# Kernel tuning notes

Hardware: AMD Instinct MI355X
Metric: run time of the kernel (lower is better)

The kernel has to match this reference:

```python
import jax, jax.numpy as jnp
import numpy as np
from jax import lax

B, CIN, COUT, H, W = 16, 256, 128, 32, 32
KD = 3   # deformable conv kernel
KU = 4
PAD = 1  # deform conv padding
EPS = 1e-5


def setup_inputs() -> dict:
    key = jax.random.key(0)
    ks = jax.random.split(key, 5)
    s3 = 1.0 / np.sqrt(CIN * KD * KD)
    s_up = 1.0 / np.sqrt(COUT * KU * KU)
    return {
        "x": jax.random.normal(ks[0], (B, CIN, H, W), jnp.float32),
        "w_off": jax.random.normal(ks[1], (3 * KD * KD, CIN, KD, KD), jnp.float32) * s3,
        "b_off": jnp.zeros((3 * KD * KD,), jnp.float32),
        "w_dcn": jax.random.normal(ks[2], (COUT, CIN, KD, KD), jnp.float32) * s3,
        "b_dcn": jnp.zeros((COUT,), jnp.float32),
        "g1": jnp.ones((COUT,), jnp.float32),
        "bt1": jnp.zeros((COUT,), jnp.float32),
        "w_up": jax.random.normal(ks[3], (COUT, COUT, KU, KU), jnp.float32) * s_up,  # torch ConvTranspose2d weight layout (in, out, kh, kw)
        "g2": jnp.ones((COUT,), jnp.float32),
        "bt2": jnp.zeros((COUT,), jnp.float32),
    }


def _conv3x3(x, w, b):
    y = lax.conv_general_dilated(x, w, (1, 1), [(1, 1), (1, 1)],
                                 dimension_numbers=("NCHW", "OIHW", "NCHW"))
    return y + b[None, :, None, None]


def _bn_relu(x, g, b):
    # training-mode BatchNorm2d: batch stats over (N, H, W), biased variance
    mu = jnp.mean(x, (0, 2, 3), keepdims=True)
    var = jnp.var(x, (0, 2, 3), keepdims=True)
    y = (x - mu) * lax.rsqrt(var + EPS)
    return jax.nn.relu(y * g[None, :, None, None] + b[None, :, None, None])


def _deform_conv(x, offset, mask, w, b):
    # modulated deformable conv v2, matching torchvision.ops.DeformConv2d
    Bb, C, Hh, Ww = x.shape
    Kk = KD * KD
    off = offset.reshape(Bb, Kk, 2, Hh, Ww)
    dy, dx = off[:, :, 0], off[:, :, 1]          # [B, Kk, H, W]
    ky, kx = jnp.meshgrid(jnp.arange(KD), jnp.arange(KD), indexing="ij")
    ky = (ky.reshape(-1) - PAD).astype(x.dtype)  # [Kk]
    kx = (kx.reshape(-1) - PAD).astype(x.dtype)
    ii = jnp.arange(Hh, dtype=x.dtype)[None, None, :, None]
    jj = jnp.arange(Ww, dtype=x.dtype)[None, None, None, :]
    py = ii + ky[None, :, None, None] + dy       # [B, Kk, H, W] sample rows
    px = jj + kx[None, :, None, None] + dx       # [B, Kk, H, W] sample cols
    y0 = jnp.floor(py)
    x0 = jnp.floor(px)
    wy = py - y0
    wx = px - x0
    HW = Hh * Ww
    x_flat = x.reshape(Bb, 1, C, HW)

    def corner(yc, xc, wgt):
        valid = (yc >= 0) & (yc <= Hh - 1) & (xc >= 0) & (xc <= Ww - 1)
        yi = jnp.clip(yc, 0, Hh - 1).astype(jnp.int32)
        xi = jnp.clip(xc, 0, Ww - 1).astype(jnp.int32)
        idx = (yi * Ww + xi).reshape(Bb, Kk, 1, HW)
        v = jnp.take_along_axis(x_flat, jnp.broadcast_to(idx, (Bb, Kk, C, HW)), axis=-1)
        wv = (wgt * valid.astype(x.dtype)).reshape(Bb, Kk, 1, HW)
        return v * wv

    samp = (corner(y0, x0, (1 - wy) * (1 - wx)) + corner(y0, x0 + 1, (1 - wy) * wx)
            + corner(y0 + 1, x0, wy * (1 - wx)) + corner(y0 + 1, x0 + 1, wy * wx))
    samp = samp * mask.reshape(Bb, Kk, 1, HW)    # [B, Kk, C, HW]
    out = jnp.einsum("bkcp,ock->bop", samp, w.reshape(w.shape[0], C, Kk))
    return out.reshape(Bb, -1, Hh, Ww) + b[None, :, None, None]


def reference(x, w_off, b_off, w_dcn, b_dcn, g1, bt1, w_up, g2, bt2):
    off = _conv3x3(x, w_off, b_off)              # [B, 27, H, W]
    Kk = KD * KD
    o1, o2, m = off[:, :Kk], off[:, Kk:2 * Kk], off[:, 2 * Kk:]
    offset = jnp.concatenate([o1, o2], axis=1)   # [B, 18, H, W], torchvision pair layout
    mask = jax.nn.sigmoid(m)
    y = _deform_conv(x, offset, mask, w_dcn, b_dcn)
    y = _bn_relu(y, g1, bt1)
    # ConvTranspose2d(k=4, s=2, p=1): conv over lhs-dilated input with flipped kernel
    w_t = jnp.flip(w_up, (2, 3)).transpose(1, 0, 2, 3)  # (out, in, kh, kw)
    p = KU - 1 - 1  # k - 1 - deconv_pad
    y = lax.conv_general_dilated(y, w_t, (1, 1), [(p, p), (p, p)],
                                 lhs_dilation=(2, 2),
                                 dimension_numbers=("NCHW", "OIHW", "NCHW"))
    return _bn_relu(y, g2, bt2)
```

## Files before the change

### kernel.cpp

```cpp
#include <hip/hip_runtime.h>
#include <hip/hip_fp16.h>
#include <math.h>

#define HW 1024
#define EPSV 1e-5f

typedef unsigned int uint;
typedef unsigned short ushort;
typedef __attribute__((ext_vector_type(8))) short short8;
typedef __attribute__((ext_vector_type(8))) _Float16 half8;
typedef __attribute__((ext_vector_type(4))) float floatx4;

static const size_t BOFF = 0;
static const size_t BD   = 36864;
static const size_t BQ   = 184320;
static const size_t XT   = 315392;
static const size_t OFFB = 2412544;
static const size_t ST1  = 2936832;
static const size_t ST2  = 2937856;
static const size_t YP   = 2941952;
static const size_t YSUM = 7136256;
static const size_t YBN  = 8184832;
static const size_t OB   = 9233408;

__device__ inline ushort f2bf(float f) {
  uint u = __builtin_bit_cast(uint, f);
  uint r = (u + 0x7FFFu + ((u >> 16) & 1u)) >> 16;
  return (ushort)r;
}
__device__ inline float b2f(ushort u) {
  return __builtin_bit_cast(float, ((uint)u) << 16);
}

__global__ __launch_bounds__(256) void prep_xt_kernel(const float* __restrict__ x,
                                                      const float* __restrict__ w_off,
                                                      const float* __restrict__ w_dcn,
                                                      const float* __restrict__ w_up,
                                                      float* __restrict__ ws) {
  __shared__ float tile[64 * 65];
  int blk = blockIdx.x;
  int tid = threadIdx.x;
  if (blk < 1024) {
    int b = blk & 15, pt = (blk >> 4) & 15, cc = blk >> 8;
    int p0 = pt * 64, c0 = cc * 64;
    int pp4 = tid & 15, ci = tid >> 4;
#pragma unroll
    for (int it = 0; it < 4; ++it) {
      int c = it * 16 + ci;
      float4 v = *(const float4*)(x + ((size_t)(b * 256 + c0 + c)) * HW + p0 + pp4 * 4);
      tile[c * 65 + pp4 * 4 + 0] = v.x;
      tile[c * 65 + pp4 * 4 + 1] = v.y;
      tile[c * 65 + pp4 * 4 + 2] = v.z;
      tile[c * 65 + pp4 * 4 + 3] = v.w;
    }
    __syncthreads();
    int cp = tid & 31, pp2 = tid >> 5;
    uint* xtu = (uint*)(ws + XT);
#pragma unroll
    for (int it = 0; it < 8; ++it) {
      int p = it * 8 + pp2;
      __half2 h = __floats2half2_rn(tile[(2 * cp) * 65 + p], tile[(2 * cp + 1) * 65 + p]);
      xtu[(size_t)(b * 1024 + p0 + p) * 128 + cc * 32 + cp] = __builtin_bit_cast(uint, h);
    }
  } else if (blk < 3488) {
    int i = (blk - 1024) * 256 + tid;
    if (i < 73728) {
      int j = i & 7;
      int lane = (i >> 3) & 63;
      int nh = (i >> 9) & 1;
      int k2 = (i >> 10) & 3;
      int cs = (i >> 12) & 1;
      int tap = i >> 13;
      int n = nh * 16 + (lane & 15);
      int c = cs * 128 + k2 * 32 + (lane >> 4) * 8 + j;
      float v = (n < 27) ? w_off[((size_t)n * 256 + c) * 9 + tap] : 0.f;
      ((__half*)(ws + BOFF))[i] = __float2half(v);
    } else if (i < 73728 + 294912) {
      int d = i - 73728;
      int oc = d / 2304; int k = d % 2304;
      int tap = k >> 8; int c = k & 255;
      ((__half*)(ws + BD))[d] = __float2half(w_dcn[((size_t)oc * 256 + c) * 9 + tap]);
    } else if (i < 73728 + 294912 + 262144) {
      int d = i - (73728 + 294912);
      int j = d & 7; int n = (d >> 3) & 127; int quad = (d >> 10) & 3;
      int kstep = (d >> 12) & 15; int par = d >> 16;
      int k = kstep * 32 + quad * 8 + j;
      int t4 = k >> 7; int c = k & 127;
      int ty = t4 >> 1, tx = t4 & 1;
      int pu = par >> 1, pv = par & 1;
      int ky = (1 - pu) + 2 * ty, kx = (1 - pv) + 2 * tx;
      float v = w_up[((size_t)c * 128 + n) * 16 + ky * 4 + kx];
      ((ushort*)(ws + BQ))[d] = f2bf(v);
    }
  } else {
    int i = (blk - 3488) * 256 + tid;
    if (i < 5120) ws[ST1 + i] = 0.f;
    else if (i < 5120 + 524288) ws[OFFB + (i - 5120)] = 0.f;
  }
}

__global__ __launch_bounds__(256) void offconv_mfma_kernel(const __half* __restrict__ xt,
                                                           const __half* __restrict__ bofr,
                                                           float* __restrict__ off) {
  __shared__ short As[102 * 132];
  int blk = blockIdx.x;
  int b = blk & 15, cs = (blk >> 4) & 1, pt = blk >> 5;
  int h = pt;
  int tid = threadIdx.x;
  int wid = tid >> 6, lane = tid & 63, lr = lane & 15, quad = lane >> 4;
  int m_w = (wid & 1) * 16, nh = wid >> 1;
  int n_w = nh * 16;
  const __half* xb = xt + (size_t)b * 1024 * 256 + cs * 128;

  for (int idx = tid; idx < 1632; idx += 256) {
    int pos = idx >> 4, seg = idx & 15;
    int r = pos / 34, jj = pos - r * 34;
    int ig = min(max(h - 1 + r, 0), 31);
    int jg = min(max(jj - 1, 0), 31);
    const float4* src = (const float4*)(xb + (size_t)(ig * 32 + jg) * 256 + seg * 8);
    *(float4*)(As + pos * 132 + seg * 8) = *src;
  }
  __syncthreads();

  floatx4 acc = (floatx4)0.f;
  int m = m_w + lr;
  const __half* bb = bofr + (size_t)lane * 8;
#pragma unroll
  for (int tap = 0; tap < 9; ++tap) {
    int ty = tap / 3, tx = tap % 3;
    bool valid = (h + ty - 1 >= 0) && (h + ty - 1 <= 31) && (m + tx - 1 >= 0) && (m + tx - 1 <= 31);
    int apos = (ty * 34 + m + tx) * 132;
#pragma unroll
    for (int k2 = 0; k2 < 4; ++k2) {
      short8 a = *(const short8*)(As + apos + k2 * 32 + quad * 8);
      short8 az = valid ? a : (short8)0;
      half8 af = __builtin_bit_cast(half8, az);
      half8 bf = *(const half8*)(bb + (size_t)((((tap * 2 + cs) * 4 + k2) * 2) + nh) * 512);
      acc = __builtin_amdgcn_mfma_f32_16x16x32_f16(af, bf, acc, 0, 0, 0);
    }
  }
  int n = n_w + lr;
#pragma unroll
  for (int r = 0; r < 4; ++r) {
    int mm = m_w + quad * 4 + r;
    atomicAdd(&off[((size_t)(b * 1024 + pt * 32 + mm)) * 32 + n], acc[r]);
  }
}

__global__ __launch_bounds__(256, 8) void deform_mfma_kernel(const __half* __restrict__ xt,
                                                             const float* __restrict__ off,
                                                             const float* __restrict__ b_off,
                                                             const __half* __restrict__ bd,
                                                             ushort* __restrict__ y_part) {
  __shared__ short As[64 * 72];
  __shared__ short Bs[128 * 72];
  int blk = blockIdx.x;
  int b = blk & 15;
  int rr = blk >> 4;
  int ptile = rr & 15, cs = rr >> 4;
  int tid = threadIdx.x;
  int wid = tid >> 6, lane = tid & 63, lr = lane & 15, quad = lane >> 4;
  int m_w = (wid & 1) * 32, n_w = (wid >> 1) * 64;
  int P0 = ptile * 64;
  int pix_l = tid >> 2, cseg = tid & 3;
  int pix = P0 + pix_l;
  int h = pix >> 5, w = pix & 31;
  const float* offb = off + (size_t)(b * 1024 + pix) * 32;
  const __half* xb = xt + (size_t)b * 1024 * 256 + cs * 64 + cseg * 16;
  int ocb = tid >> 1, seg = tid & 1;
  const __half* bdr = bd + (size_t)ocb * 2304 + cs * 64 + seg * 32;

  floatx4 acc[2][4];
#pragma unroll
  for (int mi = 0; mi < 2; ++mi)
#pragma unroll
    for (int ni = 0; ni < 4; ++ni) acc[mi][ni] = (floatx4)0.f;

#pragma unroll
  for (int tap = 0; tap < 9; ++tap) {
    float2 dn = *(const float2*)(offb + 2 * tap);
    float mr = offb[18 + tap];
    float dy = dn.x + b_off[2 * tap];
    float dx = dn.y + b_off[2 * tap + 1];
    float mraw = mr + b_off[18 + tap];
    float mm = 1.f / (1.f + __expf(-mraw));
    float py = (float)(h + tap / 3 - 1) + dy;
    float px = (float)(w + tap % 3 - 1) + dx;
    float y0f = floorf(py), x0f = floorf(px);
    float wy = py - y0f, wx = px - x0f;
    int y0 = (int)y0f, x0 = (int)x0f;
    float cw[4] = {(1.f - wy) * (1.f - wx), (1.f - wy) * wx, wy * (1.f - wx), wy * wx};
    uint4 q[4][2];
    __half2 w2[4];
#pragma unroll
    for (int t = 0; t < 4; ++t) {
      int yy = y0 + (t >> 1), xx = x0 + (t & 1);
      bool v = (yy >= 0) && (yy <= 31) && (xx >= 0) && (xx <= 31);
      int yc = min(max(yy, 0), 31), xc = min(max(xx, 0), 31);
      const uint4* xr = (const uint4*)(xb + (size_t)(yc * 32 + xc) * 256);
      q[t][0] = xr[0]; q[t][1] = xr[1];
      w2[t] = __float2half2_rn(v ? cw[t] * mm : 0.f);
    }
    const float4* gb = (const float4*)(bdr + tap * 256);
    float4 b0 = gb[0], b1 = gb[1], b2 = gb[2], b3 = gb[3];

    __half2 hacc[8];
#pragma unroll
    for (int j = 0; j < 8; ++j) hacc[j] = __float2half2_rn(0.f);
#pragma unroll
    for (int t = 0; t < 4; ++t) {
      uint qa[8] = {q[t][0].x, q[t][0].y, q[t][0].z, q[t][0].w,
                    q[t][1].x, q[t][1].y, q[t][1].z, q[t][1].w};
#pragma unroll
      for (int j = 0; j < 8; ++j)
        hacc[j] = __hfma2(w2[t], __builtin_bit_cast(__half2, qa[j]), hacc[j]);
    }
    if (tap) __syncthreads();
    {
      float4 f0, f1;
      f0.x = __builtin_bit_cast(float, hacc[0]);
      f0.y = __builtin_bit_cast(float, hacc[1]);
      f0.z = __builtin_bit_cast(float, hacc[2]);
      f0.w = __builtin_bit_cast(float, hacc[3]);
      f1.x = __builtin_bit_cast(float, hacc[4]);
      f1.y = __builtin_bit_cast(float, hacc[5]);
      f1.z = __builtin_bit_cast(float, hacc[6]);
      f1.w = __builtin_bit_cast(float, hacc[7]);
      float4* qa2 = (float4*)(As + pix_l * 72 + cseg * 16);
      qa2[0] = f0; qa2[1] = f1;
    }
    float4* qb = (float4*)(Bs + ocb * 72 + seg * 32);
    qb[0] = b0; qb[1] = b1; qb[2] = b2; qb[3] = b3;
    __syncthreads();
#pragma unroll
    for (int k2 = 0; k2 < 2; ++k2) {
      half8 af[2], bf[4];
#pragma unroll
      for (int mi = 0; mi < 2; ++mi)
        af[mi] = *(const half8*)(As + (m_w + mi * 16 + lr) * 72 + k2 * 32 + quad * 8);
#pragma unroll
      for (int ni = 0; ni < 4; ++ni)
        bf[ni] = *(const half8*)(Bs + (n_w + ni * 16 + lr) * 72 + k2 * 32 + quad * 8);
#pragma unroll
      for (int mi = 0; mi < 2; ++mi)
#pragma unroll
        for (int ni = 0; ni < 4; ++ni)
          acc[mi][ni] = __builtin_amdgcn_mfma_f32_16x16x32_f16(af[mi], bf[ni], acc[mi][ni], 0, 0, 0);
    }
  }
  ushort* yp = y_part + (size_t)cs * 2097152 + ((size_t)(b * 1024 + P0)) * 128;
#pragma unroll
  for (int mi = 0; mi < 2; ++mi) {
#pragma unroll
    for (int r = 0; r < 4; ++r) {
      int m = m_w + mi * 16 + quad * 4 + r;
      ushort* orow = yp + (size_t)m * 128;
#pragma unroll
      for (int ni = 0; ni < 4; ++ni)
        orow[n_w + ni * 16 + lr] = f2bf(acc[mi][ni][r]);
    }
  }
}

__global__ __launch_bounds__(256) void yred_kernel(const ushort* __restrict__ yp,
                                                   const float* __restrict__ b_dcn,
                                                   ushort* __restrict__ ysum,
                                                   float* __restrict__ st1) {
  int blk = blockIdx.x;
  int b = blk & 15, seg = blk >> 4;
  int tid = threadIdx.x;
  int px = tid >> 4, ocg = tid & 15;
  int lane = tid & 63, wid = tid >> 6;
  size_t idx = ((size_t)(b * 1024 + seg * 16 + px)) * 128 + ocg * 8;
  short8 p0 = *(const short8*)(yp + idx);
  short8 p1 = *(const short8*)(yp + 2097152 + idx);
  short8 p2 = *(const short8*)(yp + 4194304 + idx);
  short8 p3 = *(const short8*)(yp + 6291456 + idx);
  float s[8], q[8];
  short8 ov;
#pragma unroll
  for (int j = 0; j < 8; ++j) {
    float v = b2f((ushort)p0[j]) + b2f((ushort)p1[j]) + b2f((ushort)p2[j])
            + b2f((ushort)p3[j]) + b_dcn[ocg * 8 + j];
    ov[j] = (short)f2bf(v);
    s[j] = v; q[j] = v * v;
  }
  *(short8*)(ysum + idx) = ov;
#pragma unroll
  for (int j = 0; j < 8; ++j) {
    s[j] += __shfl_xor(s[j], 16); s[j] += __shfl_xor(s[j], 32);
    q[j] += __shfl_xor(q[j], 16); q[j] += __shfl_xor(q[j], 32);
  }
  __shared__ float red[4][256];
  if (lane < 16) {
#pragma unroll
    for (int j = 0; j < 8; ++j) {
      red[wid][lane * 8 + j] = s[j];
      red[wid][128 + lane * 8 + j] = q[j];
    }
  }
  __syncthreads();
  float tot = red[0][tid] + red[1][tid] + red[2][tid] + red[3][tid];
  atomicAdd(&st1[(blk & 3) * 256 + tid], tot);
}

__global__ __launch_bounds__(256) void deconv_mfma_kernel(const ushort* __restrict__ ysum,
                                                          const float* __restrict__ st1,
                                                          const float* __restrict__ g1,
                                                          const float* __restrict__ bt1,
                                                          const ushort* __restrict__ bq,
                                                          ushort* __restrict__ O,
                                                          float* __restrict__ st2) {
  __shared__ short Asd[102 * 132];
  __shared__ float scs[128], shs[128];
  int blk = blockIdx.x;
  int b = blk & 15, par = (blk >> 4) & 3, pt = blk >> 6;
  int pu = par >> 1, pv = par & 1;
  int tid = threadIdx.x;
  int wid = tid >> 6, lane = tid & 63, lr = lane & 15, quad = lane >> 4;
  int P0 = pt * 64;
  int h0 = pt * 2;
  const ushort* ysb = ysum + (size_t)b * 1024 * 128;

  if (tid < 128) {
    float s  = st1[tid] + st1[256 + tid] + st1[512 + tid] + st1[768 + tid];
    float sq = st1[128 + tid] + st1[384 + tid] + st1[640 + tid] + st1[896 + tid];
    float mean = s / 16384.f;
    float var = sq / 16384.f - mean * mean;
    float sc = g1[tid] * rsqrtf(var + EPSV);
    scs[tid] = sc;
    shs[tid] = fmaf(-mean, sc, bt1[tid]);
  }
  __syncthreads();

  for (int idx = tid; idx < 1632; idx += 256) {
    int pos = idx >> 4, seg = idx & 15;
    int r = pos / 34, jj = pos - r * 34;
    int ig = min(max(h0 + pu - 1 + r, 0), 31);
    int jg = min(max(pv - 1 + jj, 0), 31);
    uint4 u = *(const uint4*)(ysb + (size_t)(ig * 32 + jg) * 128 + seg * 8);
    uint words[4] = {u.x, u.y, u.z, u.w};
    uint ow[4];
    int oc0 = seg * 8;
#pragma unroll
    for (int j = 0; j < 4; ++j) {
      ushort u0 = (ushort)(words[j] & 0xFFFFu);
      ushort u1 = (ushort)(words[j] >> 16);
      int c0 = oc0 + 2 * j, c1 = oc0 + 2 * j + 1;
      float v0 = fmaxf(fmaf(b2f(u0), scs[c0], shs[c0]), 0.f);
      float v1 = fmaxf(fmaf(b2f(u1), scs[c1], shs[c1]), 0.f);
      ow[j] = (uint)f2bf(v0) | ((uint)f2bf(v1) << 16);
    }
    uint4 packed = make_uint4(ow[0], ow[1], ow[2], ow[3]);
    *(uint4*)(Asd + pos * 132 + seg * 8) = packed;
  }
  __syncthreads();

  int hh[4], ww[4];
#pragma unroll
  for (int mi = 0; mi < 4; ++mi) {
    int p = P0 + mi * 16 + lr;
    hh[mi] = p >> 5; ww[mi] = p & 31;
  }

  floatx4 acc[4][2];
#pragma unroll
  for (int mi = 0; mi < 4; ++mi)
#pragma unroll
    for (int ni = 0; ni < 2; ++ni) acc[mi][ni] = (floatx4)0.f;

  const ushort* bqb = bq + par * 65536 + quad * 1024 + (wid * 32 + lr) * 8;

#pragma unroll
  for (int tap = 0; tap < 4; ++tap) {
    int ty = tap >> 1, tx = tap & 1;
    int apos[4]; bool val[4];
#pragma unroll
    for (int mi = 0; mi < 4; ++mi) {
      int i = hh[mi] + pu - ty, j = ww[mi] + pv - tx;
      val[mi] = (i >= 0) && (i <= 31) && (j >= 0) && (j <= 31);
      int r = hh[mi] - h0 + 1 - ty;
      int jdx = ww[mi] - tx + 1;
      apos[mi] = (r * 34 + jdx) * 132;
    }
#pragma unroll
    for (int k2 = 0; k2 < 4; ++k2) {
      int kstep = tap * 4 + k2;
      int c0 = k2 * 32 + quad * 8;
      short8 bf[2];
#pragma unroll
      for (int ni = 0; ni < 2; ++ni)
        bf[ni] = *(const short8*)(bqb + kstep * 4096 + ni * 128);
      short8 af[4];
#pragma unroll
      for (int mi = 0; mi < 4; ++mi) {
        short8 a = *(const short8*)(Asd + apos[mi] + c0);
        af[mi] = val[mi] ? a : (short8)0;
      }
#pragma unroll
      for (int mi = 0; mi < 4; ++mi)
#pragma unroll
        for (int ni = 0; ni < 2; ++ni)
          acc[mi][ni] = __builtin_amdgcn_mfma_f32_16x16x32_bf16(af[mi], bf[ni], acc[mi][ni], 0, 0, 0);
    }
  }
  size_t obase = (size_t)(b * 4 + par) * 1024 * 128;
#pragma unroll
  for (int mi = 0; mi < 4; ++mi) {
#pragma unroll
    for (int r = 0; r < 4; ++r) {
      int m = mi * 16 + quad * 4 + r;
      ushort* orow = O + obase + (size_t)(P0 + m) * 128 + wid * 32;
#pragma unroll
      for (int ni = 0; ni < 2; ++ni)
        orow[ni * 16 + lr] = f2bf(acc[mi][ni][r]);
    }
  }
  float sn[2], qn[2];
#pragma unroll
  for (int ni = 0; ni < 2; ++ni) {
    float s = 0.f, q = 0.f;
#pragma unroll
    for (int mi = 0; mi < 4; ++mi)
#pragma unroll
      for (int r = 0; r < 4; ++r) {
        float v = acc[mi][ni][r];
        s += v; q = fmaf(v, v, q);
      }
    sn[ni] = s; qn[ni] = q;
  }
#pragma unroll
  for (int ni = 0; ni < 2; ++ni) {
    sn[ni] += __shfl_xor(sn[ni], 16);
    sn[ni] += __shfl_xor(sn[ni], 32);
    qn[ni] += __shfl_xor(qn[ni], 16);
    qn[ni] += __shfl_xor(qn[ni], 32);
  }
  if (lane < 16) {
    float* dst = st2 + pt * 256;
#pragma unroll
    for (int ni = 0; ni < 2; ++ni) {
      atomicAdd(&dst[wid * 32 + ni * 16 + lr], sn[ni]);
      atomicAdd(&dst[128 + wid * 32 + ni * 16 + lr], qn[ni]);
    }
  }
}

__global__ __launch_bounds__(256) void bnout_kernel(const ushort* __restrict__ O,
                                                    const float* __restrict__ st2,
                                                    const float* __restrict__ g2,
                                                    const float* __restrict__ bt2,
                                                    float* __restrict__ out) {
  __shared__ float tile[128 * 65];
  __shared__ float scs[128], shs[128];
  int blk = blockIdx.x;
  int b = blk & 15, pu = (blk >> 4) & 1, uu = blk >> 5;
  int tid = threadIdx.x;
  if (tid < 128) {
    float s = 0.f, sq = 0.f;
#pragma unroll
    for (int c = 0; c < 16; ++c) {
      s += st2[c * 256 + tid];
      sq += st2[c * 256 + 128 + tid];
    }
    float mean = s / 65536.f;
    float var = sq / 65536.f - mean * mean;
    float sc = g2[tid] * rsqrtf(var + EPSV);
    scs[tid] = sc;
    shs[tid] = fmaf(-mean, sc, bt2[tid]);
  }
  __syncthreads();
#pragma unroll
  for (int it = 0; it < 8; ++it) {
    int linear = it * 256 + tid;
    int ocg = linear & 31;
    int vv = (linear >> 5) & 31;
    int pv = linear >> 10;
    const ushort* src = O + ((size_t)(b * 4 + 2 * pu + pv) * 1024 + uu * 32 + vv) * 128 + ocg * 4;
    uint2 u = *(const uint2*)src;
    int col = 2 * vv + pv;
    int oc0 = ocg * 4;
    ushort e0 = (ushort)(u.x & 0xFFFFu), e1 = (ushort)(u.x >> 16);
    ushort e2 = (ushort)(u.y & 0xFFFFu), e3 = (ushort)(u.y >> 16);
    tile[(oc0 + 0) * 65 + col] = fmaxf(fmaf(b2f(e0), scs[oc0 + 0], shs[oc0 + 0]), 0.f);
    tile[(oc0 + 1) * 65 + col] = fmaxf(fmaf(b2f(e1), scs[oc0 + 1], shs[oc0 + 1]), 0.f);
    tile[(oc0 + 2) * 65 + col] = fmaxf(fmaf(b2f(e2), scs[oc0 + 2], shs[oc0 + 2]), 0.f);
    tile[(oc0 + 3) * 65 + col] = fmaxf(fmaf(b2f(e3), scs[oc0 + 3], shs[oc0 + 3]), 0.f);
  }
  __syncthreads();
  int row = 2 * uu + pu;
#pragma unroll
  for (int it = 0; it < 8; ++it) {
    int oc = it * 16 + (tid >> 4);
    int c4 = (tid & 15) * 4;
    float4 v;
    v.x = tile[oc * 65 + c4 + 0];
    v.y = tile[oc * 65 + c4 + 1];
    v.z = tile[oc * 65 + c4 + 2];
    v.w = tile[oc * 65 + c4 + 3];
    *(float4*)(out + ((size_t)(b * 128 + oc)) * 4096 + row * 64 + c4) = v;
  }
}

extern "C" void kernel_launch(void* const* d_in, const int* in_sizes, int n_in,
                              void* d_out, int out_size, void* d_ws, size_t ws_size,
                              hipStream_t stream) {
  const float* x     = (const float*)d_in[0];
  const float* w_off = (const float*)d_in[1];
  const float* b_off = (const float*)d_in[2];
  const float* w_dcn = (const float*)d_in[3];
  const float* b_dcn = (const float*)d_in[4];
  const float* g1    = (const float*)d_in[5];
  const float* bt1   = (const float*)d_in[6];
  const float* w_up  = (const float*)d_in[7];
  const float* g2    = (const float*)d_in[8];
  const float* bt2   = (const float*)d_in[9];
  float* ws  = (float*)d_ws;
  float* out = (float*)d_out;

  prep_xt_kernel<<<5556, 256, 0, stream>>>(x, w_off, w_dcn, w_up, ws);
  offconv_mfma_kernel<<<1024, 256, 0, stream>>>((const __half*)(ws + XT),
                                                (const __half*)(ws + BOFF), ws + OFFB);
  deform_mfma_kernel<<<1024, 256, 0, stream>>>((const __half*)(ws + XT), ws + OFFB, b_off,
                                               (const __half*)(ws + BD), (ushort*)(ws + YP));
  yred_kernel<<<1024, 256, 0, stream>>>((const ushort*)(ws + YP), b_dcn,
                                        (ushort*)(ws + YSUM), ws + ST1);
  deconv_mfma_kernel<<<1024, 256, 0, stream>>>((const ushort*)(ws + YSUM), ws + ST1, g1, bt1,
                                               (const ushort*)(ws + BQ),
                                               (ushort*)(ws + OB), ws + ST2);
  bnout_kernel<<<1024, 256, 0, stream>>>((const ushort*)(ws + OB), ws + ST2, g2, bt2, out);
}
```

Baseline: 160.2 us.

## Reorganize deform gather thread mapping and pre-pack DCN weights for coalesced loads

The bilinear gather now maps 8 threads per pixel with 8 channels each (two pixels per thread) instead of 4 threads with 16 channels, so each corner fetch becomes one 16-byte load spread across more lanes. The DCN weight matrix is repacked at prep time into a tap/channel-slice/thread-major layout so each thread reads its 64 bytes contiguously and the block's reads are fully coalesced. The launch-bounds occupancy hint of 8 is dropped, which relaxes the register cap at the cost of possibly lower occupancy.

Measured after the change: 163.1 us. No clear change (+1.9%).

```diff
diff --git a/kernel.cpp b/kernel.cpp
--- a/kernel.cpp
+++ b/kernel.cpp
@@ -77,9 +77,14 @@
       ((__half*)(ws + BOFF))[i] = __float2half(v);
     } else if (i < 73728 + 294912) {
       int d = i - 73728;
-      int oc = d / 2304; int k = d % 2304;
-      int tap = k >> 8; int c = k & 255;
-      ((__half*)(ws + BD))[d] = __float2half(w_dcn[((size_t)oc * 256 + c) * 9 + tap]);
+      int e = d & 31;
+      int t = (d >> 5) & 255;
+      int g = d >> 13;
+      int csx = g & 3;
+      int tap = g >> 2;
+      int ocb = t >> 1, seg = t & 1;
+      int c = csx * 64 + seg * 32 + e;
+      ((__half*)(ws + BD))[d] = __float2half(w_dcn[((size_t)ocb * 256 + c) * 9 + tap]);
     } else if (i < 73728 + 294912 + 262144) {
       int d = i - (73728 + 294912);
       int j = d & 7; int n = (d >> 3) & 127; int quad = (d >> 10) & 3;
@@ -147,11 +152,11 @@
   }
 }
 
-__global__ __launch_bounds__(256, 8) void deform_mfma_kernel(const __half* __restrict__ xt,
-                                                             const float* __restrict__ off,
-                                                             const float* __restrict__ b_off,
-                                                             const __half* __restrict__ bd,
-                                                             ushort* __restrict__ y_part) {
+__global__ __launch_bounds__(256) void deform_mfma_kernel(const __half* __restrict__ xt,
+                                                          const float* __restrict__ off,
+                                                          const float* __restrict__ b_off,
+                                                          const __half* __restrict__ bdF,
+                                                          ushort* __restrict__ y_part) {
   __shared__ short As[64 * 72];
   __shared__ short Bs[128 * 72];
   int blk = blockIdx.x;
@@ -162,13 +167,13 @@
   int wid = tid >> 6, lane = tid & 63, lr = lane & 15, quad = lane >> 4;
   int m_w = (wid & 1) * 32, n_w = (wid >> 1) * 64;
   int P0 = ptile * 64;
-  int pix_l = tid >> 2, cseg = tid & 3;
-  int pix = P0 + pix_l;
-  int h = pix >> 5, w = pix & 31;
-  const float* offb = off + (size_t)(b * 1024 + pix) * 32;
-  const __half* xb = xt + (size_t)b * 1024 * 256 + cs * 64 + cseg * 16;
+  int pix8 = tid >> 3, cseg8 = tid & 7;
+  const __half* xb = xt + (size_t)b * 1024 * 256 + cs * 64 + cseg8 * 8;
+  const float* offb0 = off + (size_t)(b * 1024 + P0 + pix8) * 32;
+  int hp[2], wp[2];
+  hp[0] = (P0 + pix8) >> 5;      wp[0] = (P0 + pix8) & 31;
+  hp[1] = (P0 + pix8 + 32) >> 5; wp[1] = (P0 + pix8 + 32) & 31;
   int ocb = tid >> 1, seg = tid & 1;
-  const __half* bdr = bd + (size_t)ocb * 2304 + cs * 64 + seg * 32;
 
   floatx4 acc[2][4];
 #pragma unroll
@@ -178,59 +183,61 @@
 
 #pragma unroll
   for (int tap = 0; tap < 9; ++tap) {
-    float2 dn = *(const float2*)(offb + 2 * tap);
-    float mr = offb[18 + tap];
-    float dy = dn.x + b_off[2 * tap];
-    float dx = dn.y + b_off[2 * tap + 1];
-    float mraw = mr + b_off[18 + tap];
-    float mm = 1.f / (1.f + __expf(-mraw));
-    float py = (float)(h + tap / 3 - 1) + dy;
-    float px = (float)(w + tap % 3 - 1) + dx;
-    float y0f = floorf(py), x0f = floorf(px);
-    float wy = py - y0f, wx = px - x0f;
-    int y0 = (int)y0f, x0 = (int)x0f;
-    float cw[4] = {(1.f - wy) * (1.f - wx), (1.f - wy) * wx, wy * (1.f - wx), wy * wx};
-    uint4 q[4][2];
-    __half2 w2[4];
-#pragma unroll
-    for (int t = 0; t < 4; ++t) {
-      int yy = y0 + (t >> 1), xx = x0 + (t & 1);
-      bool v = (yy >= 0) && (yy <= 31) && (xx >= 0) && (xx <= 31);
-      int yc = min(max(yy, 0), 31), xc = min(max(xx, 0), 31);
-      const uint4* xr = (const uint4*)(xb + (size_t)(yc * 32 + xc) * 256);
-      q[t][0] = xr[0]; q[t][1] = xr[1];
-      w2[t] = __float2half2_rn(v ? cw[t] * mm : 0.f);
-    }
-    const float4* gb = (const float4*)(bdr + tap * 256);
-    float4 b0 = gb[0], b1 = gb[1], b2 = gb[2], b3 = gb[3];
-
-    __half2 hacc[8];
-#pragma unroll
-    for (int j = 0; j < 8; ++j) hacc[j] = __float2half2_rn(0.f);
-#pragma unroll
-    for (int t = 0; t < 4; ++t) {
-      uint qa[8] = {q[t][0].x, q[t][0].y, q[t][0].z, q[t][0].w,
-                    q[t][1].x, q[t][1].y, q[t][1].z, q[t][1].w};
-#pragma unroll
-      for (int j = 0; j < 8; ++j)
-        hacc[j] = __hfma2(w2[t], __builtin_bit_cast(__half2, qa[j]), hacc[j]);
+    int ty = tap / 3, tx = tap % 3;
+    uint4 q[2][4];
+    __half2 w2[2][4];
+#pragma unroll
+    for (int pp = 0; pp < 2; ++pp) {
+      const float* ob = offb0 + pp * 1024;
+      float2 dn = *(const float2*)(ob + 2 * tap);
+      float mraw = ob[18 + tap] + b_off[18 + tap];
+      float dy = dn.x + b_off[2 * tap];
+      float dx = dn.y + b_off[2 * tap + 1];
+      float mm = 1.f / (1.f + __expf(-mraw));
+      float py = (float)(hp[pp] + ty - 1) + dy;
+      float px = (float)(wp[pp] + tx - 1) + dx;
+      float y0f = floorf(py), x0f = floorf(px);
+      float wy = py - y0f, wx = px - x0f;
+      int y0 = (int)y0f, x0 = (int)x0f;
+      float cw[4] = {(1.f - wy) * (1.f - wx), (1.f - wy) * wx, wy * (1.f - wx), wy * wx};
+#pragma unroll
+      for (int t = 0; t < 4; ++t) {
+        int yy = y0 + (t >> 1), xx = x0 + (t & 1);
+        bool v = (yy >= 0) && (yy <= 31) && (xx >= 0) && (xx <= 31);
+        int yc = min(max(yy, 0), 31), xc = min(max(xx, 0), 31);
+        q[pp][t] = *(const uint4*)(xb + (size_t)(yc * 32 + xc) * 256);
+        w2[pp][t] = __float2half2_rn(v ? cw[t] * mm : 0.f);
+      }
+    }
+    const __half* bsrc = bdF + ((size_t)(tap * 4 + cs) * 256 + tid) * 32;
+    float4 bv0 = ((const float4*)bsrc)[0];
+    float4 bv1 = ((const float4*)bsrc)[1];
+    float4 bv2 = ((const float4*)bsrc)[2];
+    float4 bv3 = ((const float4*)bsrc)[3];
+
+    float4 f[2];
+#pragma unroll
+    for (int pp = 0; pp < 2; ++pp) {
+      __half2 hacc[4];
+#pragma unroll
+      for (int j = 0; j < 4; ++j) hacc[j] = __float2half2_rn(0.f);
+#pragma unroll
+      for (int t = 0; t < 4; ++t) {
+        uint qa[4] = {q[pp][t].x, q[pp][t].y, q[pp][t].z, q[pp][t].w};
+#pragma unroll
+        for (int j = 0; j < 4; ++j)
+          hacc[j] = __hfma2(w2[pp][t], __builtin_bit_cast(__half2, qa[j]), hacc[j]);
+      }
+      f[pp].x = __builtin_bit_cast(float, hacc[0]);
+      f[pp].y = __builtin_bit_cast(float, hacc[1]);
+      f[pp].z = __builtin_bit_cast(float, hacc[2]);
+      f[pp].w = __builtin_bit_cast(float, hacc[3]);
     }
     if (tap) __syncthreads();
-    {
-      float4 f0, f1;
-      f0.x = __builtin_bit_cast(float, hacc[0]);
-      f0.y = __builtin_bit_cast(float, hacc[1]);
-      f0.z = __builtin_bit_cast(float, hacc[2]);
-      f0.w = __builtin_bit_cast(float, hacc[3]);
-      f1.x = __builtin_bit_cast(float, hacc[4]);
-      f1.y = __builtin_bit_cast(float, hacc[5]);
-      f1.z = __builtin_bit_cast(float, hacc[6]);
-      f1.w = __builtin_bit_cast(float, hacc[7]);
-      float4* qa2 = (float4*)(As + pix_l * 72 + cseg * 16);
-      qa2[0] = f0; qa2[1] = f1;
-    }
+    *(float4*)(As + pix8 * 72 + cseg8 * 8) = f[0];
+    *(float4*)(As + (pix8 + 32) * 72 + cseg8 * 8) = f[1];
     float4* qb = (float4*)(Bs + ocb * 72 + seg * 32);
-    qb[0] = b0; qb[1] = b1; qb[2] = b2; qb[3] = b3;
+    qb[0] = bv0; qb[1] = bv1; qb[2] = bv2; qb[3] = bv3;
     __syncthreads();
 #pragma unroll
     for (int k2 = 0; k2 < 2; ++k2) {
```
